# Performance work log

Measured on AMD Instinct MI355X. Metric: run time of the kernel, lower is better.

The kernel has to match this reference:

```python
import jax, jax.numpy as jnp
import numpy as np

B, M_CONS, F = 32768, 32, 4
N_ITERS = 400  # fixed-iteration projected-gradient on the dual (Q = I so dual is a box-constrained QP)


def setup_inputs() -> dict:
    key = jax.random.key(0)
    kA, kx, kv, ks = jax.random.split(key, 4)
    A = jax.random.normal(kA, (B, M_CONS, F), dtype=jnp.float32)
    x = jax.random.normal(kx, (B, F), dtype=jnp.float32)
    # Construct b so the polyhedron {w : 2 A w <= b} is nonempty (v0 feasible)
    # with small slacks so many constraints are active (nontrivial QP).
    v0 = jax.random.normal(kv, (B, F), dtype=jnp.float32)
    slack = jnp.abs(jax.random.normal(ks, (B, M_CONS), dtype=jnp.float32)) * 0.1
    b = 2.0 * jnp.einsum('bmf,bf->bm', A, v0) + slack
    return {"A": A, "x": x, "b": b}


def reference(A, x, b):
    # Original: min_z 0.5 z^T Q z + p^T z  s.t. G z <= b, with Q = I (2F x 2F),
    #   G = [A | A]  (cat along feature dim), p = -[x; -x] = [-x; x].
    # Dual (Q = I): min_{lam >= 0} lam^T (G G^T) lam / 1 ... f(lam) = lam^T M lam + q^T lam
    #   with M = 0.5 * 2 * G G^T handled below; z* = -(p + G^T lam*).
    f = x.shape[-1]
    G = jnp.concatenate([A, A], axis=2)            # [B, m, 2F]
    p = jnp.concatenate([-x, x], axis=1)           # [B, 2F]
    M = jnp.einsum('bmi,bni->bmn', G, G)           # [B, m, m] = G G^T
    q = jnp.einsum('bmi,bi->bm', G, p) + b         # [B, m]
    # dual objective: 0.5 lam^T M lam + q^T lam, grad = M lam + q, lam >= 0
    # Lipschitz bound for step size: ||M||_2 <= ||M||_F
    L = jnp.sqrt(jnp.sum(M * M, axis=(1, 2))) + 1e-6   # [B]
    alpha = (1.0 / L)[:, None]                     # [B, 1]
    lam0 = jnp.zeros_like(b)

    def step(lam, _):
        grad = jnp.einsum('bmn,bn->bm', M, lam) + q
        lam = jax.nn.relu(lam - alpha * grad)
        return lam, None

    lam, _ = jax.lax.scan(step, lam0, None, length=N_ITERS)
    z = -(p + jnp.einsum('bmi,bm->bi', G, lam))    # [B, 2F]
    # (y[0:F] + y[F:]) / 2
    return (z[:, :f] + z[:, f:]) * 0.5
```

## Files before the change

kernel.cpp:

```cpp
#include <hip/hip_runtime.h>


#define QP_ITERS 400

typedef float v2f __attribute__((ext_vector_type(2)));

template <int CTRL>
__device__ __forceinline__ float dpp_add(float v) {
    return v + __int_as_float(
        __builtin_amdgcn_update_dpp(0, __float_as_int(v), CTRL, 0xF, 0xF, true));
}

__device__ __forceinline__ float pair_sum(float v) {
    return dpp_add<0xB1>(v);
}

__global__ void __launch_bounds__(256)
__attribute__((amdgpu_waves_per_eu(1, 1)))
qp_pgd_kernel(
        const float* __restrict__ A,
        const float* __restrict__ b,
        float* __restrict__ out,
        int nprob) {
    int t = blockIdx.x * blockDim.x + threadIdx.x;
    int p = t >> 1;
    int j = t & 1;
    if (p >= nprob) return;

    const float4* Ar = reinterpret_cast<const float4*>(A + (size_t)p * 128 + (size_t)j * 64);
    const float4* br = reinterpret_cast<const float4*>(b + (size_t)p * 32 + (size_t)j * 16);

    float ax[16], ay[16], az[16], aw[16];
#pragma unroll
    for (int k = 0; k < 16; ++k) {
        float4 r = Ar[k];
        ax[k] = r.x; ay[k] = r.y; az[k] = r.z; aw[k] = r.w;
    }
    float bb[16];
#pragma unroll
    for (int k = 0; k < 4; ++k) {
        float4 bv = br[k];
        bb[4 * k + 0] = bv.x; bb[4 * k + 1] = bv.y;
        bb[4 * k + 2] = bv.z; bb[4 * k + 3] = bv.w;
    }

    float s00 = 0.f, s01 = 0.f, s02 = 0.f, s03 = 0.f;
    float s11 = 0.f, s12 = 0.f, s13 = 0.f;
    float s22 = 0.f, s23 = 0.f, s33 = 0.f;
#pragma unroll
    for (int k = 0; k < 16; ++k) {
        s00 = fmaf(ax[k], ax[k], s00);
        s01 = fmaf(ax[k], ay[k], s01);
        s02 = fmaf(ax[k], az[k], s02);
        s03 = fmaf(ax[k], aw[k], s03);
        s11 = fmaf(ay[k], ay[k], s11);
        s12 = fmaf(ay[k], az[k], s12);
        s13 = fmaf(ay[k], aw[k], s13);
        s22 = fmaf(az[k], az[k], s22);
        s23 = fmaf(az[k], aw[k], s23);
        s33 = fmaf(aw[k], aw[k], s33);
    }
    s00 = pair_sum(s00); s01 = pair_sum(s01); s02 = pair_sum(s02); s03 = pair_sum(s03);
    s11 = pair_sum(s11); s12 = pair_sum(s12); s13 = pair_sum(s13);
    s22 = pair_sum(s22); s23 = pair_sum(s23); s33 = pair_sum(s33);
    float ssq = s00 * s00 + s11 * s11 + s22 * s22 + s33 * s33
              + 2.f * (s01 * s01 + s02 * s02 + s03 * s03
                     + s12 * s12 + s13 * s13 + s23 * s23);
    float L = 2.f * sqrtf(ssq) + 1e-6f;
    float alpha = 1.f / L;
    float sc = sqrtf(2.f * alpha);
    float inv_sc = 1.f / sc;

    v2f axp[8], ayp[8], azp[8], awp[8], mcp[8], lamp[8];
#pragma unroll
    for (int i = 0; i < 8; ++i) {
        axp[i] = (v2f){ax[2 * i] * sc, ax[2 * i + 1] * sc};
        ayp[i] = (v2f){ay[2 * i] * sc, ay[2 * i + 1] * sc};
        azp[i] = (v2f){az[2 * i] * sc, az[2 * i + 1] * sc};
        awp[i] = (v2f){aw[2 * i] * sc, aw[2 * i + 1] * sc};
        mcp[i] = (v2f){-alpha * bb[2 * i], -alpha * bb[2 * i + 1]};
        lamp[i] = (v2f){0.f, 0.f};
    }

#pragma unroll 2
    for (int it = 0; it < QP_ITERS; ++it) {
        v2f a0 = (v2f){0.f, 0.f}, a1 = (v2f){0.f, 0.f};
        v2f a2 = (v2f){0.f, 0.f}, a3 = (v2f){0.f, 0.f};
#pragma unroll
        for (int i = 0; i < 8; ++i) {
            a0 = __builtin_elementwise_fma(axp[i], lamp[i], a0);
            a1 = __builtin_elementwise_fma(ayp[i], lamp[i], a1);
            a2 = __builtin_elementwise_fma(azp[i], lamp[i], a2);
            a3 = __builtin_elementwise_fma(awp[i], lamp[i], a3);
        }
        float u0 = pair_sum(a0.x + a0.y);
        float u1 = pair_sum(a1.x + a1.y);
        float u2 = pair_sum(a2.x + a2.y);
        float u3 = pair_sum(a3.x + a3.y);
        v2f U0 = (v2f){-u0, -u0}, U1 = (v2f){-u1, -u1};
        v2f U2 = (v2f){-u2, -u2}, U3 = (v2f){-u3, -u3};
        const v2f z2 = (v2f){0.f, 0.f};
#pragma unroll
        for (int i = 0; i < 8; ++i) {
            v2f tt = lamp[i] + mcp[i];
            tt = __builtin_elementwise_fma(axp[i], U0, tt);
            tt = __builtin_elementwise_fma(ayp[i], U1, tt);
            tt = __builtin_elementwise_fma(azp[i], U2, tt);
            tt = __builtin_elementwise_fma(awp[i], U3, tt);
            lamp[i] = __builtin_elementwise_max(tt, z2);
        }
    }

    v2f a0 = (v2f){0.f, 0.f}, a1 = (v2f){0.f, 0.f};
    v2f a2 = (v2f){0.f, 0.f}, a3 = (v2f){0.f, 0.f};
#pragma unroll
    for (int i = 0; i < 8; ++i) {
        a0 = __builtin_elementwise_fma(axp[i], lamp[i], a0);
        a1 = __builtin_elementwise_fma(ayp[i], lamp[i], a1);
        a2 = __builtin_elementwise_fma(azp[i], lamp[i], a2);
        a3 = __builtin_elementwise_fma(awp[i], lamp[i], a3);
    }
    float u0 = pair_sum(a0.x + a0.y);
    float u1 = pair_sum(a1.x + a1.y);
    float u2 = pair_sum(a2.x + a2.y);
    float u3 = pair_sum(a3.x + a3.y);
    float lo = (j == 0) ? u0 : u2;
    float hi = (j == 0) ? u1 : u3;
    float2 o = make_float2(-lo * inv_sc, -hi * inv_sc);
    *reinterpret_cast<float2*>(out + (size_t)p * 4 + (size_t)j * 2) = o;
}

extern "C" void kernel_launch(void* const* d_in, const int* in_sizes, int n_in,
                              void* d_out, int out_size, void* d_ws, size_t ws_size,
                              hipStream_t stream) {
    const float* A = (const float*)d_in[0];
    const float* b = (const float*)d_in[2];
    float* out = (float*)d_out;

    int nprob = in_sizes[2] / 32;
    int threads = nprob * 2;
    dim3 block(256);
    dim3 grid((threads + 255) / 256);
    hipLaunchKernelGGL(qp_pgd_kernel, grid, block, 0, stream, A, b, out, nprob);
}
```

Measured before the change: 87.38 us.

## Fuse lambda update with next-iteration reduction and use scalar FMAs

Merges the projection step and the G^T·lambda accumulation into a single loop, so the reduction for iteration k+1 is accumulated while lambda is updated in iteration k. The cross-lane pair sum moves to the top of the loop. Packed two-wide float vectors are replaced with scalar fmaf, and the unroll-2 pragma is dropped. This removes a separate pass over the constraint registers but may lose dual-issue packed FMA throughput.

```diff
diff --git a/kernel.cpp b/kernel.cpp
--- a/kernel.cpp
+++ b/kernel.cpp
@@ -2,8 +2,6 @@
 
 
 #define QP_ITERS 400
-
-typedef float v2f __attribute__((ext_vector_type(2)));
 
 template <int CTRL>
 __device__ __forceinline__ float dpp_add(float v) {
@@ -13,6 +11,10 @@
 
 __device__ __forceinline__ float pair_sum(float v) {
     return dpp_add<0xB1>(v);
+}
+
+__device__ __forceinline__ float fneg_bits(float v) {
+    return __int_as_float(__float_as_int(v) ^ 0x80000000);
 }
 
 __global__ void __launch_bounds__(256)
@@ -71,61 +73,42 @@
     float sc = sqrtf(2.f * alpha);
     float inv_sc = 1.f / sc;
 
-    v2f axp[8], ayp[8], azp[8], awp[8], mcp[8], lamp[8];
+    float mc[16], lam[16];
 #pragma unroll
-    for (int i = 0; i < 8; ++i) {
-        axp[i] = (v2f){ax[2 * i] * sc, ax[2 * i + 1] * sc};
-        ayp[i] = (v2f){ay[2 * i] * sc, ay[2 * i + 1] * sc};
-        azp[i] = (v2f){az[2 * i] * sc, az[2 * i + 1] * sc};
-        awp[i] = (v2f){aw[2 * i] * sc, aw[2 * i + 1] * sc};
-        mcp[i] = (v2f){-alpha * bb[2 * i], -alpha * bb[2 * i + 1]};
-        lamp[i] = (v2f){0.f, 0.f};
+    for (int k = 0; k < 16; ++k) {
+        ax[k] *= sc; ay[k] *= sc; az[k] *= sc; aw[k] *= sc;
+        mc[k] = -alpha * bb[k];
+        lam[k] = 0.f;
     }
 
-#pragma unroll 2
+    float u0 = 0.f, u1 = 0.f, u2 = 0.f, u3 = 0.f;
+
     for (int it = 0; it < QP_ITERS; ++it) {
-        v2f a0 = (v2f){0.f, 0.f}, a1 = (v2f){0.f, 0.f};
-        v2f a2 = (v2f){0.f, 0.f}, a3 = (v2f){0.f, 0.f};
+        float U0 = pair_sum(u0), U1 = pair_sum(u1);
+        float U2 = pair_sum(u2), U3 = pair_sum(u3);
+        float n0 = fneg_bits(U0), n1 = fneg_bits(U1);
+        float n2 = fneg_bits(U2), n3 = fneg_bits(U3);
+        u0 = 0.f; u1 = 0.f; u2 = 0.f; u3 = 0.f;
 #pragma unroll
-        for (int i = 0; i < 8; ++i) {
-            a0 = __builtin_elementwise_fma(axp[i], lamp[i], a0);
-            a1 = __builtin_elementwise_fma(ayp[i], lamp[i], a1);
-            a2 = __builtin_elementwise_fma(azp[i], lamp[i], a2);
-            a3 = __builtin_elementwise_fma(awp[i], lamp[i], a3);
-        }
-        float u0 = pair_sum(a0.x + a0.y);
-        float u1 = pair_sum(a1.x + a1.y);
-        float u2 = pair_sum(a2.x + a2.y);
-        float u3 = pair_sum(a3.x + a3.y);
-        v2f U0 = (v2f){-u0, -u0}, U1 = (v2f){-u1, -u1};
-        v2f U2 = (v2f){-u2, -u2}, U3 = (v2f){-u3, -u3};
-        const v2f z2 = (v2f){0.f, 0.f};
-#pragma unroll
-        for (int i = 0; i < 8; ++i) {
-            v2f tt = lamp[i] + mcp[i];
-            tt = __builtin_elementwise_fma(axp[i], U0, tt);
-            tt = __builtin_elementwise_fma(ayp[i], U1, tt);
-            tt = __builtin_elementwise_fma(azp[i], U2, tt);
-            tt = __builtin_elementwise_fma(awp[i], U3, tt);
-            lamp[i] = __builtin_elementwise_max(tt, z2);
+        for (int k = 0; k < 16; ++k) {
+            float tt = lam[k] + mc[k];
+            tt = fmaf(ax[k], n0, tt);
+            tt = fmaf(ay[k], n1, tt);
+            tt = fmaf(az[k], n2, tt);
+            tt = fmaf(aw[k], n3, tt);
+            float l = fmaxf(tt, 0.f);
+            lam[k] = l;
+            u0 = fmaf(ax[k], l, u0);
+            u1 = fmaf(ay[k], l, u1);
+            u2 = fmaf(az[k], l, u2);
+            u3 = fmaf(aw[k], l, u3);
         }
     }
 
-    v2f a0 = (v2f){0.f, 0.f}, a1 = (v2f){0.f, 0.f};
-    v2f a2 = (v2f){0.f, 0.f}, a3 = (v2f){0.f, 0.f};
-#pragma unroll
-    for (int i = 0; i < 8; ++i) {
-        a0 = __builtin_elementwise_fma(axp[i], lamp[i], a0);
-        a1 = __builtin_elementwise_fma(ayp[i], lamp[i], a1);
-        a2 = __builtin_elementwise_fma(azp[i], lamp[i], a2);
-        a3 = __builtin_elementwise_fma(awp[i], lamp[i], a3);
-    }
-    float u0 = pair_sum(a0.x + a0.y);
-    float u1 = pair_sum(a1.x + a1.y);
-    float u2 = pair_sum(a2.x + a2.y);
-    float u3 = pair_sum(a3.x + a3.y);
-    float lo = (j == 0) ? u0 : u2;
-    float hi = (j == 0) ? u1 : u3;
+    float U0 = pair_sum(u0), U1 = pair_sum(u1);
+    float U2 = pair_sum(u2), U3 = pair_sum(u3);
+    float lo = (j == 0) ? U0 : U2;
+    float hi = (j == 0) ? U1 : U3;
     float2 o = make_float2(-lo * inv_sc, -hi * inv_sc);
     *reinterpret_cast<float2*>(out + (size_t)p * 4 + (size_t)j * 2) = o;
 }
```

Result: slower. 105.7 us (+21.0%).
